# Performance work log

Hardware: AMD Instinct MI355X
Metric: run time of the kernel (lower is better)

The kernel has to match this reference:

```python
import jax, jax.numpy as jnp
import numpy as np

IN_CH, OUT_CH, K, DIL = 64, 128, 3, 8

def setup_inputs() -> dict:
    key = jax.random.key(0)
    k1, k2, k3 = jax.random.split(key, 3)
    x = jax.random.normal(k1, (16, IN_CH, 128, 128), dtype=jnp.float32)
    # xavier_normal-like init for W
    fan_in, fan_out = IN_CH * K * K, OUT_CH * K * K
    std = (2.0 / (fan_in + fan_out)) ** 0.5
    W = jax.random.normal(k2, (OUT_CH, IN_CH, K, K), dtype=jnp.float32) * std
    b = jax.random.normal(k3, (OUT_CH,), dtype=jnp.float32)
    return {"x": x, "W": W, "b": b}

def reference(x, W, b):
    pad = DIL * (K // 2)  # circular halo so output spatial size == input
    xp = jnp.pad(x, ((0, 0), (0, 0), (pad, pad), (pad, pad)), mode="wrap")
    y = jax.lax.conv_general_dilated(
        xp, W,
        window_strides=(1, 1),
        padding="VALID",
        rhs_dilation=(DIL, DIL),
        dimension_numbers=("NCHW", "OIHW", "NCHW"),
    )
    return y + b[None, :, None, None]
```

## Files before the change

### kernel.cpp

```cpp
#include <hip/hip_runtime.h>

#define IN_CH 64
#define OUT_CH 128
#define HW 128
#define KTAPS 9
#define ROWB 16384

typedef __bf16 bf16x8 __attribute__((ext_vector_type(8)));
typedef float f32x16 __attribute__((ext_vector_type(16)));
typedef float f32x4 __attribute__((ext_vector_type(4)));

__device__ __forceinline__ unsigned f2bf(float f) {
    unsigned u = __builtin_bit_cast(unsigned, f);
    return (u + 0x7FFFu + ((u >> 16) & 1u)) >> 16;
}

__device__ __forceinline__ unsigned cvt_pk_bf16(float lo, float hi) {
    unsigned r;
    asm("v_cvt_pk_bf16_f32 %0, %1, %2" : "=v"(r) : "v"(lo), "v"(hi));
    return r;
}

__device__ __forceinline__ int swz(int r) { return ((r ^ (r >> 3)) & 7) << 4; }

__global__ void wprep_kernel(const float* __restrict__ W, unsigned short* __restrict__ Wl) {
    int i = blockIdx.x * blockDim.x + threadIdx.x;
    if (i >= OUT_CH * IN_CH * KTAPS) return;
    int p  = i / 36864;
    int r  = i % 36864;
    int t  = r >> 12;
    int r2 = r & 4095;
    int m  = r2 >> 11;
    int ks = (r2 >> 9) & 3;
    int l  = (r2 >> 3) & 63;
    int e  = r2 & 7;
    int oc = p * 64 + m * 32 + (l & 31);
    int ic = ks * 16 + (l >> 5) * 8 + e;
    int kh = t / 3, kw = t % 3;
    Wl[i] = (unsigned short)f2bf(W[((oc * IN_CH + ic) * 3 + kh) * 3 + kw]);
}

__global__ __launch_bounds__(512, 6) void conv_kernel_f(
    const float* __restrict__ x, const unsigned short* __restrict__ Wl,
    const float* __restrict__ bias, float* __restrict__ y)
{
    __shared__ __align__(16) unsigned char xsB[3 * ROWB];

    int bid = blockIdx.x;
    int sb  = (bid & 7) * 256 + (bid >> 3);
    int n = sb >> 7, h = sb & 127;
    int tid = threadIdx.x;
    int wid = tid >> 6, lane = tid & 63;

    #pragma unroll
    for (int g = 0; g < 3; ++g) {
        int q   = g * 512 + tid;
        int w4  = q & 31;
        int ic4 = (q >> 5) & 15;
        int kh  = q >> 9;
        int srow = (h + kh * 8 + 120) & 127;
        const float* xp = x + (((n * IN_CH + ic4 * 4) * HW + srow) * HW + w4 * 4);
        f32x4 v[4];
        #pragma unroll
        for (int j = 0; j < 4; ++j)
            v[j] = *reinterpret_cast<const f32x4*>(xp + j * (HW * HW));
        #pragma unroll
        for (int j2 = 0; j2 < 4; ++j2) {
            int w = w4 * 4 + j2;
            uint2 pk;
            pk.x = cvt_pk_bf16(v[0][j2], v[1][j2]);
            pk.y = cvt_pk_bf16(v[2][j2], v[3][j2]);
            *reinterpret_cast<uint2*>(xsB + kh * ROWB + ((w * 128 + ic4 * 8) ^ swz(w))) = pk;
        }
    }
    __syncthreads();

    int wr = wid >> 1, wc = wid & 1;
    int l31 = lane & 31, lhi = lane >> 5;
    int p = wr >> 1, m = wr & 1;

    const bf16x8* Ab = reinterpret_cast<const bf16x8*>(Wl)
                     + p * (9 * 512) + m * 256 + lane;

    f32x16 acc[2];
    #pragma unroll
    for (int bq = 0; bq < 2; ++bq)
        #pragma unroll
        for (int r = 0; r < 16; ++r) acc[bq][r] = 0.0f;

    #pragma unroll
    for (int t = 0; t < 9; ++t) {
        bf16x8 aCur[4];
        #pragma unroll
        for (int ks = 0; ks < 4; ++ks) aCur[ks] = Ab[t * 512 + ks * 64];

        int kh = t / 3, kw = t % 3;
        int xc0 = (wc * 64 + l31 + 8 * kw - 8) & 127;
        int xc1 = (xc0 + 32) & 127;
        int b0base = kh * ROWB + xc0 * 128 + lhi * 16, s0 = swz(xc0);
        int b1base = kh * ROWB + xc1 * 128 + lhi * 16, s1 = swz(xc1);
        #pragma unroll
        for (int ks = 0; ks < 4; ++ks) {
            bf16x8 b0 = *reinterpret_cast<const bf16x8*>(xsB + ((b0base + ks * 32) ^ s0));
            bf16x8 b1 = *reinterpret_cast<const bf16x8*>(xsB + ((b1base + ks * 32) ^ s1));
            acc[0] = __builtin_amdgcn_mfma_f32_32x32x16_bf16(aCur[ks], b0, acc[0], 0, 0, 0);
            acc[1] = __builtin_amdgcn_mfma_f32_32x32x16_bf16(aCur[ks], b1, acc[1], 0, 0, 0);
        }
    }

    int outbase = (n * OUT_CH) * HW * HW + h * HW;
    #pragma unroll
    for (int bq = 0; bq < 2; ++bq) {
        int wcol = wc * 64 + bq * 32 + l31;
        #pragma unroll
        for (int reg = 0; reg < 16; ++reg) {
            int oc = wr * 32 + (reg & 3) + 8 * (reg >> 2) + 4 * lhi;
            y[outbase + oc * HW * HW + wcol] = acc[bq][reg] + bias[oc];
        }
    }
}

extern "C" void kernel_launch(void* const* d_in, const int* in_sizes, int n_in,
                              void* d_out, int out_size, void* d_ws, size_t ws_size,
                              hipStream_t stream) {
    const float* x = (const float*)d_in[0];
    const float* W = (const float*)d_in[1];
    const float* b = (const float*)d_in[2];
    float* y = (float*)d_out;

    unsigned short* Wl = (unsigned short*)d_ws;

    hipLaunchKernelGGL(wprep_kernel, dim3((OUT_CH * IN_CH * KTAPS + 255) / 256), dim3(256), 0, stream, W, Wl);
    hipLaunchKernelGGL(conv_kernel_f, dim3(16 * HW), dim3(512), 0, stream, x, Wl, b, y);
}
```

Measured before the change: 63.69 us.

## Stage weight tiles in LDS via async global_load_lds with double buffering

Weights are now loaded per tap into a double-buffered LDS region with global_load_lds, prefetching the next tap while the current one is computed, instead of each wave reading its A fragments straight from global memory. The wprep layout is reordered so that each tap is one contiguous 16 KB block. LDS use rises from 48 KB to 80 KB, the occupancy hint drops from 6 to 4 blocks, and a __syncthreads per tap is added. There is no explicit vmcnt wait before the barrier, which may be a correctness risk with async LDS loads.

```diff
diff --git a/kernel.cpp b/kernel.cpp
--- a/kernel.cpp
+++ b/kernel.cpp
@@ -5,6 +5,7 @@
 #define HW 128
 #define KTAPS 9
 #define ROWB 16384
+#define ATAP 16384
 
 typedef __bf16 bf16x8 __attribute__((ext_vector_type(8)));
 typedef float f32x16 __attribute__((ext_vector_type(16)));
@@ -23,34 +24,50 @@
 
 __device__ __forceinline__ int swz(int r) { return ((r ^ (r >> 3)) & 7) << 4; }
 
+__device__ __forceinline__ void gload_lds16(const void* g, void* l) {
+    __builtin_amdgcn_global_load_lds(
+        (const __attribute__((address_space(1))) unsigned int*)g,
+        (__attribute__((address_space(3))) unsigned int*)l, 16, 0, 0);
+}
+
 __global__ void wprep_kernel(const float* __restrict__ W, unsigned short* __restrict__ Wl) {
     int i = blockIdx.x * blockDim.x + threadIdx.x;
     if (i >= OUT_CH * IN_CH * KTAPS) return;
-    int p  = i / 36864;
-    int r  = i % 36864;
-    int t  = r >> 12;
-    int r2 = r & 4095;
-    int m  = r2 >> 11;
-    int ks = (r2 >> 9) & 3;
-    int l  = (r2 >> 3) & 63;
-    int e  = r2 & 7;
-    int oc = p * 64 + m * 32 + (l & 31);
+    int t  = i >> 13;
+    int r  = i & 8191;
+    int c  = r >> 3;
+    int e  = r & 7;
+    int l  = c & 63;
+    int q2 = c >> 6;
+    int ks = q2 & 3;
+    int pm = q2 >> 2;
+    int oc = pm * 32 + (l & 31);
     int ic = ks * 16 + (l >> 5) * 8 + e;
     int kh = t / 3, kw = t % 3;
     Wl[i] = (unsigned short)f2bf(W[((oc * IN_CH + ic) * 3 + kh) * 3 + kw]);
 }
 
-__global__ __launch_bounds__(512, 6) void conv_kernel_f(
+__global__ __launch_bounds__(512, 4) void conv_kernel_f(
     const float* __restrict__ x, const unsigned short* __restrict__ Wl,
     const float* __restrict__ bias, float* __restrict__ y)
 {
     __shared__ __align__(16) unsigned char xsB[3 * ROWB];
+    __shared__ __align__(16) unsigned char xsA[2 * ATAP];
 
     int bid = blockIdx.x;
     int sb  = (bid & 7) * 256 + (bid >> 3);
     int n = sb >> 7, h = sb & 127;
     int tid = threadIdx.x;
     int wid = tid >> 6, lane = tid & 63;
+
+    {
+        const unsigned char* asrc = (const unsigned char*)Wl;
+        #pragma unroll
+        for (int j = 0; j < 2; ++j) {
+            int off = wid * 2048 + j * 1024;
+            gload_lds16(asrc + off + lane * 16, xsA + off);
+        }
+    }
 
     #pragma unroll
     for (int g = 0; g < 3; ++g) {
@@ -77,10 +94,6 @@
 
     int wr = wid >> 1, wc = wid & 1;
     int l31 = lane & 31, lhi = lane >> 5;
-    int p = wr >> 1, m = wr & 1;
-
-    const bf16x8* Ab = reinterpret_cast<const bf16x8*>(Wl)
-                     + p * (9 * 512) + m * 256 + lane;
 
     f32x16 acc[2];
     #pragma unroll
@@ -90,10 +103,16 @@
 
     #pragma unroll
     for (int t = 0; t < 9; ++t) {
-        bf16x8 aCur[4];
-        #pragma unroll
-        for (int ks = 0; ks < 4; ++ks) aCur[ks] = Ab[t * 512 + ks * 64];
-
+        if (t < 8) {
+            const unsigned char* asrc = (const unsigned char*)Wl + (t + 1) * ATAP;
+            unsigned char* adst = xsA + ((t + 1) & 1) * ATAP;
+            #pragma unroll
+            for (int j = 0; j < 2; ++j) {
+                int off = wid * 2048 + j * 1024;
+                gload_lds16(asrc + off + lane * 16, adst + off);
+            }
+        }
+        const unsigned char* At = xsA + (t & 1) * ATAP + wr * 4096;
         int kh = t / 3, kw = t % 3;
         int xc0 = (wc * 64 + l31 + 8 * kw - 8) & 127;
         int xc1 = (xc0 + 32) & 127;
@@ -101,11 +120,13 @@
         int b1base = kh * ROWB + xc1 * 128 + lhi * 16, s1 = swz(xc1);
         #pragma unroll
         for (int ks = 0; ks < 4; ++ks) {
+            bf16x8 a  = *reinterpret_cast<const bf16x8*>(At + ks * 1024 + lane * 16);
             bf16x8 b0 = *reinterpret_cast<const bf16x8*>(xsB + ((b0base + ks * 32) ^ s0));
             bf16x8 b1 = *reinterpret_cast<const bf16x8*>(xsB + ((b1base + ks * 32) ^ s1));
-            acc[0] = __builtin_amdgcn_mfma_f32_32x32x16_bf16(aCur[ks], b0, acc[0], 0, 0, 0);
-            acc[1] = __builtin_amdgcn_mfma_f32_32x32x16_bf16(aCur[ks], b1, acc[1], 0, 0, 0);
+            acc[0] = __builtin_amdgcn_mfma_f32_32x32x16_bf16(a, b0, acc[0], 0, 0, 0);
+            acc[1] = __builtin_amdgcn_mfma_f32_32x32x16_bf16(a, b1, acc[1], 0, 0, 0);
         }
+        if (t < 8) __syncthreads();
     }
 
     int outbase = (n * OUT_CH) * HW * HW + h * HW;
```

Result: slower. 70.59 us (+10.8%).

## Compute two output rows per block sharing dilated input rows in LDS

Applied to the files above, without the earlier changes.

Each block now computes two output rows spaced 8 apart (h0 and h0+8). The input rows they need overlap, so the block stages 4 input rows in LDS instead of 3 for one row, which cuts global input loads and bf16 conversion per output row. Each wave now covers 64 output channels for one of the two rows, with 4 accumulator tiles instead of 2. The grid is halved and launch bounds drop to 3 blocks per SM, trading occupancy for more register and LDS use and more MFMA work per block.

```diff
diff --git a/kernel.cpp b/kernel.cpp
--- a/kernel.cpp
+++ b/kernel.cpp
@@ -40,25 +40,27 @@
     Wl[i] = (unsigned short)f2bf(W[((oc * IN_CH + ic) * 3 + kh) * 3 + kw]);
 }
 
-__global__ __launch_bounds__(512, 6) void conv_kernel_f(
+__global__ __launch_bounds__(512, 3) void conv_kernel_f(
     const float* __restrict__ x, const unsigned short* __restrict__ Wl,
     const float* __restrict__ bias, float* __restrict__ y)
 {
-    __shared__ __align__(16) unsigned char xsB[3 * ROWB];
+    __shared__ __align__(16) unsigned char xsB[4 * ROWB];
 
     int bid = blockIdx.x;
-    int sb  = (bid & 7) * 256 + (bid >> 3);
-    int n = sb >> 7, h = sb & 127;
+    int sb  = (bid & 7) * 128 + (bid >> 3);
+    int n   = sb >> 6;
+    int pp  = sb & 63;
+    int h0  = (pp >> 3) * 16 + (pp & 7);
     int tid = threadIdx.x;
     int wid = tid >> 6, lane = tid & 63;
 
     #pragma unroll
-    for (int g = 0; g < 3; ++g) {
+    for (int g = 0; g < 4; ++g) {
         int q   = g * 512 + tid;
         int w4  = q & 31;
         int ic4 = (q >> 5) & 15;
-        int kh  = q >> 9;
-        int srow = (h + kh * 8 + 120) & 127;
+        int r   = q >> 9;
+        int srow = (h0 + r * 8 + 120) & 127;
         const float* xp = x + (((n * IN_CH + ic4 * 4) * HW + srow) * HW + w4 * 4);
         f32x4 v[4];
         #pragma unroll
@@ -70,52 +72,65 @@
             uint2 pk;
             pk.x = cvt_pk_bf16(v[0][j2], v[1][j2]);
             pk.y = cvt_pk_bf16(v[2][j2], v[3][j2]);
-            *reinterpret_cast<uint2*>(xsB + kh * ROWB + ((w * 128 + ic4 * 8) ^ swz(w))) = pk;
+            *reinterpret_cast<uint2*>(xsB + r * ROWB + ((w * 128 + ic4 * 8) ^ swz(w))) = pk;
         }
     }
     __syncthreads();
 
-    int wr = wid >> 1, wc = wid & 1;
+    int hq = wid >> 2;
+    int wp = (wid >> 1) & 1;
+    int wc = wid & 1;
     int l31 = lane & 31, lhi = lane >> 5;
-    int p = wr >> 1, m = wr & 1;
 
-    const bf16x8* Ab = reinterpret_cast<const bf16x8*>(Wl)
-                     + p * (9 * 512) + m * 256 + lane;
+    const bf16x8* Ab0 = reinterpret_cast<const bf16x8*>(Wl) + 0 * (9 * 512) + wp * 256 + lane;
+    const bf16x8* Ab1 = reinterpret_cast<const bf16x8*>(Wl) + 1 * (9 * 512) + wp * 256 + lane;
 
-    f32x16 acc[2];
+    f32x16 acc[2][2];
     #pragma unroll
-    for (int bq = 0; bq < 2; ++bq)
+    for (int qs = 0; qs < 2; ++qs)
         #pragma unroll
-        for (int r = 0; r < 16; ++r) acc[bq][r] = 0.0f;
+        for (int bq = 0; bq < 2; ++bq)
+            #pragma unroll
+            for (int r = 0; r < 16; ++r) acc[qs][bq][r] = 0.0f;
 
     #pragma unroll
     for (int t = 0; t < 9; ++t) {
-        bf16x8 aCur[4];
+        bf16x8 a0[4], a1[4];
         #pragma unroll
-        for (int ks = 0; ks < 4; ++ks) aCur[ks] = Ab[t * 512 + ks * 64];
-
+        for (int ks = 0; ks < 4; ++ks) {
+            a0[ks] = Ab0[t * 512 + ks * 64];
+            a1[ks] = Ab1[t * 512 + ks * 64];
+        }
         int kh = t / 3, kw = t % 3;
+        int br  = (kh + hq) * ROWB;
         int xc0 = (wc * 64 + l31 + 8 * kw - 8) & 127;
         int xc1 = (xc0 + 32) & 127;
-        int b0base = kh * ROWB + xc0 * 128 + lhi * 16, s0 = swz(xc0);
-        int b1base = kh * ROWB + xc1 * 128 + lhi * 16, s1 = swz(xc1);
+        int b0base = br + xc0 * 128 + lhi * 16, s0 = swz(xc0);
+        int b1base = br + xc1 * 128 + lhi * 16, s1 = swz(xc1);
         #pragma unroll
         for (int ks = 0; ks < 4; ++ks) {
             bf16x8 b0 = *reinterpret_cast<const bf16x8*>(xsB + ((b0base + ks * 32) ^ s0));
             bf16x8 b1 = *reinterpret_cast<const bf16x8*>(xsB + ((b1base + ks * 32) ^ s1));
-            acc[0] = __builtin_amdgcn_mfma_f32_32x32x16_bf16(aCur[ks], b0, acc[0], 0, 0, 0);
-            acc[1] = __builtin_amdgcn_mfma_f32_32x32x16_bf16(aCur[ks], b1, acc[1], 0, 0, 0);
+            acc[0][0] = __builtin_amdgcn_mfma_f32_32x32x16_bf16(a0[ks], b0, acc[0][0], 0, 0, 0);
+            acc[0][1] = __builtin_amdgcn_mfma_f32_32x32x16_bf16(a0[ks], b1, acc[0][1], 0, 0, 0);
+            acc[1][0] = __builtin_amdgcn_mfma_f32_32x32x16_bf16(a1[ks], b0, acc[1][0], 0, 0, 0);
+            acc[1][1] = __builtin_amdgcn_mfma_f32_32x32x16_bf16(a1[ks], b1, acc[1][1], 0, 0, 0);
         }
     }
 
-    int outbase = (n * OUT_CH) * HW * HW + h * HW;
+    int hout = h0 + hq * 8;
+    int outbase = (n * OUT_CH) * HW * HW + hout * HW;
     #pragma unroll
-    for (int bq = 0; bq < 2; ++bq) {
-        int wcol = wc * 64 + bq * 32 + l31;
+    for (int qs = 0; qs < 2; ++qs) {
+        int ocb = qs * 64 + wp * 32;
         #pragma unroll
-        for (int reg = 0; reg < 16; ++reg) {
-            int oc = wr * 32 + (reg & 3) + 8 * (reg >> 2) + 4 * lhi;
-            y[outbase + oc * HW * HW + wcol] = acc[bq][reg] + bias[oc];
+        for (int bq = 0; bq < 2; ++bq) {
+            int wcol = wc * 64 + bq * 32 + l31;
+            #pragma unroll
+            for (int reg = 0; reg < 16; ++reg) {
+                int oc = ocb + (reg & 3) + 8 * (reg >> 2) + 4 * lhi;
+                y[outbase + oc * HW * HW + wcol] = acc[qs][bq][reg] + bias[oc];
+            }
         }
     }
 }
@@ -131,5 +146,5 @@
     unsigned short* Wl = (unsigned short*)d_ws;
 
     hipLaunchKernelGGL(wprep_kernel, dim3((OUT_CH * IN_CH * KTAPS + 255) / 256), dim3(256), 0, stream, W, Wl);
-    hipLaunchKernelGGL(conv_kernel_f, dim3(16 * HW), dim3(512), 0, stream, x, Wl, b, y);
+    hipLaunchKernelGGL(conv_kernel_f, dim3(1024), dim3(512), 0, stream, x, Wl, b, y);
 }
```

After: 68.92 us. +8.2%, slower.

## Double-buffer weight fragment loads across taps with manual vmcnt waits

Applied to the files above, without the earlier changes.

Weight fragments for the MFMA A operand are now loaded with inline-asm global loads into two register sets. The loads for the next tap are issued while the current tap computes, and the first tap's loads are issued before the input staging. Explicit s_waitcnt vmcnt and sched_barrier control when each set must be ready, to hide global/L2 latency behind the MFMAs. Launch bounds drop from 6 to 5 blocks per CU to make room for the extra registers. This risks lower occupancy and fragile correctness, because the compiler is unaware of the asynchronous asm loads.

```diff
diff --git a/kernel.cpp b/kernel.cpp
--- a/kernel.cpp
+++ b/kernel.cpp
@@ -40,7 +40,33 @@
     Wl[i] = (unsigned short)f2bf(W[((oc * IN_CH + ic) * 3 + kh) * 3 + kw]);
 }
 
-__global__ __launch_bounds__(512, 6) void conv_kernel_f(
+#define ISSUE_A(B0, B1, B2, B3, T) do {                                              \
+    const char* _pp = (const char*)Ab + (T) * 8192;                                  \
+    asm volatile("global_load_dwordx4 %0, %1, off"             : "=v"(B0) : "v"(_pp)); \
+    asm volatile("global_load_dwordx4 %0, %1, off offset:1024" : "=v"(B1) : "v"(_pp)); \
+    asm volatile("global_load_dwordx4 %0, %1, off offset:2048" : "=v"(B2) : "v"(_pp)); \
+    asm volatile("global_load_dwordx4 %0, %1, off offset:3072" : "=v"(B3) : "v"(_pp)); \
+} while (0)
+
+#define TAP_BODY(A0_, A1_, A2_, A3_, T, WAITSTR) do {                                \
+    constexpr int _kh = (T) / 3, _kw = (T) % 3;                                      \
+    int _xc0 = (wc * 64 + l31 + 8 * _kw - 8) & 127;                                  \
+    int _xc1 = (_xc0 + 32) & 127;                                                    \
+    int _b0 = _kh * ROWB + _xc0 * 128 + lhi * 16, _s0 = swz(_xc0);                   \
+    int _b1 = _kh * ROWB + _xc1 * 128 + lhi * 16, _s1 = swz(_xc1);                   \
+    asm volatile(WAITSTR);                                                           \
+    __builtin_amdgcn_sched_barrier(0);                                               \
+    const bf16x8 _A[4] = {A0_, A1_, A2_, A3_};                                       \
+    _Pragma("unroll")                                                                \
+    for (int ks = 0; ks < 4; ++ks) {                                                 \
+        bf16x8 _vb0 = *reinterpret_cast<const bf16x8*>(xsB + ((_b0 + ks * 32) ^ _s0)); \
+        bf16x8 _vb1 = *reinterpret_cast<const bf16x8*>(xsB + ((_b1 + ks * 32) ^ _s1)); \
+        acc[0] = __builtin_amdgcn_mfma_f32_32x32x16_bf16(_A[ks], _vb0, acc[0], 0, 0, 0); \
+        acc[1] = __builtin_amdgcn_mfma_f32_32x32x16_bf16(_A[ks], _vb1, acc[1], 0, 0, 0); \
+    }                                                                                \
+} while (0)
+
+__global__ __launch_bounds__(512, 5) void conv_kernel_f(
     const float* __restrict__ x, const unsigned short* __restrict__ Wl,
     const float* __restrict__ bias, float* __restrict__ y)
 {
@@ -51,6 +77,16 @@
     int n = sb >> 7, h = sb & 127;
     int tid = threadIdx.x;
     int wid = tid >> 6, lane = tid & 63;
+
+    int wr = wid >> 1, wc = wid & 1;
+    int l31 = lane & 31, lhi = lane >> 5;
+    int p = wr >> 1, m = wr & 1;
+
+    const bf16x8* Ab = reinterpret_cast<const bf16x8*>(Wl)
+                     + p * (9 * 512) + m * 256 + lane;
+
+    bf16x8 aE0, aE1, aE2, aE3, aO0, aO1, aO2, aO3;
+    ISSUE_A(aE0, aE1, aE2, aE3, 0);
 
     #pragma unroll
     for (int g = 0; g < 3; ++g) {
@@ -75,38 +111,29 @@
     }
     __syncthreads();
 
-    int wr = wid >> 1, wc = wid & 1;
-    int l31 = lane & 31, lhi = lane >> 5;
-    int p = wr >> 1, m = wr & 1;
-
-    const bf16x8* Ab = reinterpret_cast<const bf16x8*>(Wl)
-                     + p * (9 * 512) + m * 256 + lane;
-
     f32x16 acc[2];
     #pragma unroll
     for (int bq = 0; bq < 2; ++bq)
         #pragma unroll
         for (int r = 0; r < 16; ++r) acc[bq][r] = 0.0f;
 
-    #pragma unroll
-    for (int t = 0; t < 9; ++t) {
-        bf16x8 aCur[4];
-        #pragma unroll
-        for (int ks = 0; ks < 4; ++ks) aCur[ks] = Ab[t * 512 + ks * 64];
-
-        int kh = t / 3, kw = t % 3;
-        int xc0 = (wc * 64 + l31 + 8 * kw - 8) & 127;
-        int xc1 = (xc0 + 32) & 127;
-        int b0base = kh * ROWB + xc0 * 128 + lhi * 16, s0 = swz(xc0);
-        int b1base = kh * ROWB + xc1 * 128 + lhi * 16, s1 = swz(xc1);
-        #pragma unroll
-        for (int ks = 0; ks < 4; ++ks) {
-            bf16x8 b0 = *reinterpret_cast<const bf16x8*>(xsB + ((b0base + ks * 32) ^ s0));
-            bf16x8 b1 = *reinterpret_cast<const bf16x8*>(xsB + ((b1base + ks * 32) ^ s1));
-            acc[0] = __builtin_amdgcn_mfma_f32_32x32x16_bf16(aCur[ks], b0, acc[0], 0, 0, 0);
-            acc[1] = __builtin_amdgcn_mfma_f32_32x32x16_bf16(aCur[ks], b1, acc[1], 0, 0, 0);
-        }
-    }
+    ISSUE_A(aO0, aO1, aO2, aO3, 1);
+    TAP_BODY(aE0, aE1, aE2, aE3, 0, "s_waitcnt vmcnt(4)");
+    ISSUE_A(aE0, aE1, aE2, aE3, 2);
+    TAP_BODY(aO0, aO1, aO2, aO3, 1, "s_waitcnt vmcnt(4)");
+    ISSUE_A(aO0, aO1, aO2, aO3, 3);
+    TAP_BODY(aE0, aE1, aE2, aE3, 2, "s_waitcnt vmcnt(4)");
+    ISSUE_A(aE0, aE1, aE2, aE3, 4);
+    TAP_BODY(aO0, aO1, aO2, aO3, 3, "s_waitcnt vmcnt(4)");
+    ISSUE_A(aO0, aO1, aO2, aO3, 5);
+    TAP_BODY(aE0, aE1, aE2, aE3, 4, "s_waitcnt vmcnt(4)");
+    ISSUE_A(aE0, aE1, aE2, aE3, 6);
+    TAP_BODY(aO0, aO1, aO2, aO3, 5, "s_waitcnt vmcnt(4)");
+    ISSUE_A(aO0, aO1, aO2, aO3, 7);
+    TAP_BODY(aE0, aE1, aE2, aE3, 6, "s_waitcnt vmcnt(4)");
+    ISSUE_A(aE0, aE1, aE2, aE3, 8);
+    TAP_BODY(aO0, aO1, aO2, aO3, 7, "s_waitcnt vmcnt(4)");
+    TAP_BODY(aE0, aE1, aE2, aE3, 8, "s_waitcnt vmcnt(0)");
 
     int outbase = (n * OUT_CH) * HW * HW + h * HW;
     #pragma unroll
```

After: 61.22 us (median of 3 runs). 1.04x faster.
